# Kernel tuning notes

Hardware: AMD Instinct MI355X
Metric: run time of the kernel (lower is better)

## Reference

```python
import jax, jax.numpy as jnp
import numpy as np
from jax import lax

B, C, H, W = 8, 192, 128, 128
NUM_HEADS = 4
EPS = 1e-12  # torch F.normalize eps


def setup_inputs() -> dict:
    key = jax.random.key(0)
    ks = jax.random.split(key, 5)
    s = 0.05
    x = jax.random.normal(ks[0], (B, C, H, W), dtype=jnp.float32)
    w_qkv = jax.random.normal(ks[1], (3 * C, C), dtype=jnp.float32) * s      # 1x1 conv, no bias
    w_dw = jax.random.normal(ks[2], (3 * C, 1, 3, 3), dtype=jnp.float32) * s  # depthwise 3x3
    temperature = jnp.ones((1, NUM_HEADS, 1, 1), dtype=jnp.float32)
    w_out = jax.random.normal(ks[3], (C, C), dtype=jnp.float32) * s          # 1x1 conv, no bias
    return {"x": x, "w_qkv": w_qkv, "w_dw": w_dw, "temperature": temperature, "w_out": w_out}


def _l2_normalize(t):
    # matches torch F.normalize(dim=-1): t / max(||t||_2, eps)
    n = jnp.sqrt(jnp.sum(t * t, axis=-1, keepdims=True))
    return t / jnp.maximum(n, EPS)


def reference(x, w_qkv, w_dw, temperature, w_out):
    b, c, h, w = x.shape
    hd = c // NUM_HEADS
    # 1x1 pointwise conv (no bias)
    qkv = jnp.einsum('bchw,oc->bohw', x, w_qkv)
    # depthwise 3x3 conv, padding=1, groups=3c
    qkv = lax.conv_general_dilated(
        qkv, w_dw, window_strides=(1, 1), padding='SAME',
        feature_group_count=3 * c,
        dimension_numbers=('NCHW', 'OIHW', 'NCHW'))
    q, k, v = jnp.split(qkv, 3, axis=1)
    # [b, heads, head_dim, h*w]
    q = q.reshape(b, NUM_HEADS, hd, h * w)
    k = k.reshape(b, NUM_HEADS, hd, h * w)
    v = v.reshape(b, NUM_HEADS, hd, h * w)
    q = _l2_normalize(q)
    k = _l2_normalize(k)
    # channel attention: [b, heads, hd, hd]
    attn = jax.nn.softmax(jnp.einsum('bhcn,bhdn->bhcd', q, k) * temperature, axis=-1)
    out = jnp.einsum('bhcd,bhdn->bhcn', attn, v).reshape(b, c, h, w)
    out = jnp.einsum('bchw,oc->bohw', out, w_out)
    return out
```

## Files before the change

kernel.cpp:

```cpp
#include <hip/hip_runtime.h>
#include <hip/hip_bf16.h>

typedef unsigned short u16;
typedef unsigned int u32;

constexpr int kHW  = 16384;
constexpr int kC   = 192;
constexpr int kC3  = 576;
constexpr int kHD  = 48;
constexpr int kB   = 8;
constexpr int kSCH = 16;

typedef __attribute__((ext_vector_type(8))) short bfx8;
typedef __attribute__((ext_vector_type(4))) float fx4;

__device__ __forceinline__ float bfu2f(u32 u) { return __uint_as_float(u << 16); }
__device__ __forceinline__ u16 f2bfu(float f) {
  u32 x = __float_as_uint(f);
  return (u16)((x + 0x7fffu + ((x >> 16) & 1u)) >> 16);
}
__device__ __forceinline__ u32 pack2(float a, float b) {
  union { __hip_bfloat162 h; u32 u; } cv;
  cv.h = __float22bfloat162_rn(make_float2(a, b));
  return cv.u;
}

__global__ __launch_bounds__(256) void cast_f32_bf16(
    const float* __restrict__ in, u16* __restrict__ out, int n) {
  int i = blockIdx.x * 256 + threadIdx.x;
  if (i < n) out[i] = f2bfu(in[i]);
}

template <bool IN_F32, bool OUT_BF16>
__global__ __launch_bounds__(256) void gemm_cn(
    const u16* __restrict__ Abase, long aStride,
    const void* __restrict__ Bbase, long bStride,
    void* __restrict__ OutBase, long oStride, int nOB) {
  const int nwg = (int)gridDim.x;
  const int wg = ((int)blockIdx.x & 7) * (nwg >> 3) + ((int)blockIdx.x >> 3);
  const int o0 = (wg % nOB) * 64;
  const int rest = wg / nOB;
  const int n0 = (rest & 63) * 256;
  const int b  = rest >> 6;

  const int t = threadIdx.x;
  const int lane = t & 63, wv = t >> 6;
  const int fr = lane & 15, fg = lane >> 4;

  __shared__ u16 As[64 * 64];
  __shared__ __align__(16) u32 Bs[32 * 260];

  const u16* A = Abase + (size_t)b * aStride;

  fx4 acc[4][4];
#pragma unroll
  for (int m = 0; m < 4; ++m)
#pragma unroll
    for (int n = 0; n < 4; ++n) acc[m][n] = (fx4){0.f, 0.f, 0.f, 0.f};

  for (int k0 = 0; k0 < kC; k0 += 64) {
    if (k0) __syncthreads();
#pragma unroll
    for (int i = 0; i < 2; ++i) {
      int idx = t + i * 256;
      int row = idx >> 3, sl = idx & 7;
      uint4 v = *(const uint4*)(A + (size_t)(o0 + row) * kC + k0 + sl * 8);
      *(uint4*)(As + row * 64 + ((sl ^ (row & 7)) * 8)) = v;
    }
    if constexpr (IN_F32) {
      const float* Bg = (const float*)Bbase + (size_t)b * bStride;
#pragma unroll
      for (int i = 0; i < 8; ++i) {
        int p = i * 4 + wv;
        int k = k0 + 2 * p;
        const float* s0 = Bg + (size_t)k * kHW + n0 + lane * 4;
        float4 a = *(const float4*)s0;
        float4 c = *(const float4*)(s0 + (size_t)kHW);
        *(uint4*)(&Bs[p * 260 + lane * 4]) = make_uint4(
            pack2(a.x, c.x), pack2(a.y, c.y), pack2(a.z, c.z), pack2(a.w, c.w));
      }
    } else {
      const u16* Bg = (const u16*)Bbase + (size_t)b * bStride;
#pragma unroll
      for (int i = 0; i < 8; ++i) {
        int p = i * 4 + wv;
        int k = k0 + 2 * p;
        const u16* s0 = Bg + (size_t)k * kHW + n0 + lane * 4;
        uint2 a = *(const uint2*)s0;
        uint2 c = *(const uint2*)(s0 + (size_t)kHW);
        u32 w0 = (a.x & 0xffffu) | (c.x << 16);
        u32 w1 = (a.x >> 16)     | (c.x & 0xffff0000u);
        u32 w2 = (a.y & 0xffffu) | (c.y << 16);
        u32 w3 = (a.y >> 16)     | (c.y & 0xffff0000u);
        *(uint4*)(&Bs[p * 260 + lane * 4]) = make_uint4(w0, w1, w2, w3);
      }
    }
    __syncthreads();
#pragma unroll
    for (int ks = 0; ks < 2; ++ks) {
      bfx8 af[4], bf[4];
#pragma unroll
      for (int m = 0; m < 4; ++m) {
        int row = m * 16 + fr;
        af[m] = *(const bfx8*)(As + row * 64 + (((ks * 4 + fg) ^ (row & 7)) * 8));
      }
#pragma unroll
      for (int nf = 0; nf < 4; ++nf) {
        int base = (ks * 16 + fg * 4) * 260 + wv * 64 + nf * 16 + fr;
        union { uint4 u; bfx8 f; } cv;
        cv.u = make_uint4(Bs[base], Bs[base + 260], Bs[base + 520], Bs[base + 780]);
        bf[nf] = cv.f;
      }
#pragma unroll
      for (int m = 0; m < 4; ++m)
#pragma unroll
        for (int n = 0; n < 4; ++n)
          acc[m][n] = __builtin_amdgcn_mfma_f32_16x16x32_bf16(af[m], bf[n], acc[m][n], 0, 0, 0);
    }
  }

  if constexpr (OUT_BF16) {
    u16* O = (u16*)OutBase + (size_t)b * oStride;
#pragma unroll
    for (int m = 0; m < 4; ++m)
#pragma unroll
      for (int n = 0; n < 4; ++n) {
        int col = n0 + wv * 64 + n * 16 + fr;
#pragma unroll
        for (int r = 0; r < 4; ++r)
          O[(size_t)(o0 + m * 16 + fg * 4 + r) * kHW + col] = f2bfu(acc[m][n][r]);
      }
  } else {
    float* O = (float*)OutBase + (size_t)b * oStride;
#pragma unroll
    for (int m = 0; m < 4; ++m)
#pragma unroll
      for (int n = 0; n < 4; ++n) {
        int col = n0 + wv * 64 + n * 16 + fr;
#pragma unroll
        for (int r = 0; r < 4; ++r)
          O[(size_t)(o0 + m * 16 + fg * 4 + r) * kHW + col] = acc[m][n][r];
      }
  }
}

__device__ __forceinline__ void load_row3(const u16* __restrict__ plane, int hh,
                                          int w8, float v[10]) {
  uint4 m = make_uint4(0u, 0u, 0u, 0u);
  if ((unsigned)hh <= 127u) m = *(const uint4*)(plane + hh * 128 + w8 * 8);
  u32 left  = __shfl_up(m.w >> 16, 1);
  u32 right = __shfl_down(m.x & 0xffffu, 1);
  v[1] = bfu2f(m.x & 0xffffu); v[2] = bfu2f(m.x >> 16);
  v[3] = bfu2f(m.y & 0xffffu); v[4] = bfu2f(m.y >> 16);
  v[5] = bfu2f(m.z & 0xffffu); v[6] = bfu2f(m.z >> 16);
  v[7] = bfu2f(m.w & 0xffffu); v[8] = bfu2f(m.w >> 16);
  v[0] = (w8 > 0)  ? bfu2f(left)  : 0.f;
  v[9] = (w8 < 15) ? bfu2f(right) : 0.f;
}

__global__ __launch_bounds__(256) void dwconv3x3_v3(
    const u16* __restrict__ in, const float* __restrict__ wdw,
    u16* __restrict__ out, float* __restrict__ ssqp) {
  const int bc = blockIdx.x;
  const int ch = bc % kC3;
  const int t = threadIdx.x;
  const int w8 = t & 15;
  const int h0 = (t >> 4) * 8;
  const u16* p = in + (size_t)bc * kHW;
  float wt[9];
#pragma unroll
  for (int j = 0; j < 9; ++j) wt[j] = wdw[ch * 9 + j];

  float v[3][10];
  load_row3(p, h0 - 1, w8, v[0]);
  load_row3(p, h0,     w8, v[1]);
  float ssq = 0.f;
  u16* op = out + (size_t)bc * kHW + h0 * 128 + w8 * 8;
#pragma unroll
  for (int r = 0; r < 8; ++r) {
    load_row3(p, h0 + r + 1, w8, v[(r + 2) % 3]);
    const float* r0 = v[r % 3];
    const float* r1 = v[(r + 1) % 3];
    const float* r2 = v[(r + 2) % 3];
    float o[8];
#pragma unroll
    for (int j = 0; j < 8; ++j) {
      o[j] = wt[0] * r0[j] + wt[1] * r0[j + 1] + wt[2] * r0[j + 2]
           + wt[3] * r1[j] + wt[4] * r1[j + 1] + wt[5] * r1[j + 2]
           + wt[6] * r2[j] + wt[7] * r2[j + 1] + wt[8] * r2[j + 2];
      ssq += o[j] * o[j];
    }
    *(uint4*)(op + r * 128) = make_uint4(pack2(o[0], o[1]), pack2(o[2], o[3]),
                                         pack2(o[4], o[5]), pack2(o[6], o[7]));
  }
  if (ch < 2 * kC) {
#pragma unroll
    for (int d = 1; d < 64; d <<= 1) ssq += __shfl_xor(ssq, d);
    __shared__ float red[4];
    if ((t & 63) == 0) red[t >> 6] = ssq;
    __syncthreads();
    if (t == 0) ssqp[bc] = red[0] + red[1] + red[2] + red[3];
  }
}

__global__ __launch_bounds__(256) void qk_mfma_lds(
    const u16* __restrict__ qkv2, float* __restrict__ Spart) {
  const int chunk = blockIdx.x;
  const int bh = blockIdx.y;
  const int b = bh >> 2, hh = bh & 3;
  const u16* qp = qkv2 + (size_t)(b * kC3 + hh * kHD) * kHW;
  const u16* kp = qp + (size_t)kC * kHW;

  __shared__ u16 smem[24576];
  u16* qs = smem;
  u16* ks = smem + 12288;
  float* sred = (float*)smem;

  const int t = threadIdx.x;
  const int wv = t >> 6, lane = t & 63;
  const int fr = lane & 15, fg = lane >> 4;

  fx4 acc[3][3];
#pragma unroll
  for (int i = 0; i < 3; ++i)
#pragma unroll
    for (int j = 0; j < 3; ++j) acc[i][j] = (fx4){0.f, 0.f, 0.f, 0.f};

  for (int round = 0; round < 4; ++round) {
    if (round) __syncthreads();
    const int nb = chunk * 1024 + round * 256;
#pragma unroll
    for (int j = 0; j < 6; ++j) {
      int idx = t + j * 256;
      int c = idx >> 5, sl = idx & 31;
      *(uint4*)(qs + c * 256 + ((sl ^ (c & 31)) * 8)) =
          *(const uint4*)(qp + (size_t)c * kHW + nb + sl * 8);
      *(uint4*)(ks + c * 256 + ((sl ^ (c & 31)) * 8)) =
          *(const uint4*)(kp + (size_t)c * kHW + nb + sl * 8);
    }
    __syncthreads();
#pragma unroll
    for (int s = 0; s < 2; ++s) {
      const int slot = wv * 8 + s * 4 + fg;
      bfx8 aq[3], ak[3];
#pragma unroll
      for (int tt = 0; tt < 3; ++tt) {
        int c = tt * 16 + fr;
        aq[tt] = *(const bfx8*)(qs + c * 256 + ((slot ^ (c & 31)) * 8));
        ak[tt] = *(const bfx8*)(ks + c * 256 + ((slot ^ (c & 31)) * 8));
      }
#pragma unroll
      for (int i = 0; i < 3; ++i)
#pragma unroll
        for (int j = 0; j < 3; ++j)
          acc[i][j] = __builtin_amdgcn_mfma_f32_16x16x32_bf16(aq[i], ak[j], acc[i][j], 0, 0, 0);
    }
  }

  __syncthreads();
  float* my = sred + wv * 2400;
#pragma unroll
  for (int i = 0; i < 3; ++i)
#pragma unroll
    for (int j = 0; j < 3; ++j)
#pragma unroll
      for (int r = 0; r < 4; ++r)
        my[(i * 16 + fg * 4 + r) * 50 + j * 16 + fr] = acc[i][j][r];
  __syncthreads();
  float* Sp = Spart + ((size_t)chunk * 32 + bh) * (kHD * kHD);
  for (int p = t; p < kHD * kHD; p += 256) {
    int idx = (p / kHD) * 50 + (p % kHD);
    Sp[p] = sred[idx] + sred[2400 + idx] + sred[4800 + idx] + sred[7200 + idx];
  }
}

__global__ __launch_bounds__(256) void attn_softmax(
    const float* __restrict__ Spart, const float* __restrict__ ssqp,
    const float* __restrict__ temp, float* __restrict__ attn) {
  const int bh = blockIdx.x, b = bh >> 2, hh = bh & 3;
  const int t = threadIdx.x;
  __shared__ float S[kHD * kHD];
  __shared__ float qn[kHD], kinv[kHD];
  for (int p = t; p < kHD * kHD; p += 256) {
    float s = 0.f;
#pragma unroll
    for (int c = 0; c < kSCH; ++c) s += Spart[((size_t)c * 32 + bh) * (kHD * kHD) + p];
    S[p] = s;
  }
  if (t < 48) {
    qn[t] = sqrtf(ssqp[b * kC3 + hh * kHD + t]);
  } else if (t < 96) {
    kinv[t - 48] = 1.f / fmaxf(sqrtf(ssqp[b * kC3 + kC + hh * kHD + (t - 48)]), 1e-12f);
  }
  __syncthreads();
  if (t < 48) {
    const float T = temp[hh];
    const float sqr = T / fmaxf(qn[t], 1e-12f);
    float m = -3.4e38f;
    for (int d = 0; d < kHD; ++d) {
      float v = S[t * kHD + d] * sqr * kinv[d];
      S[t * kHD + d] = v;
      m = fmaxf(m, v);
    }
    float sum = 0.f;
    for (int d = 0; d < kHD; ++d) {
      float e = expf(S[t * kHD + d] - m);
      S[t * kHD + d] = e;
      sum += e;
    }
    const float inv = 1.f / sum;
    float* A = attn + (size_t)bh * (kHD * kHD) + t * kHD;
    for (int d = 0; d < kHD; ++d) A[d] = S[t * kHD + d] * inv;
  }
}

__global__ __launch_bounds__(256) void make_m(
    const float* __restrict__ wout, const float* __restrict__ attn, u16* __restrict__ M) {
  int g = blockIdx.x * 256 + threadIdx.x;
  if (g >= kB * kC * kC) return;
  int j = g % kC;
  int o = (g / kC) % kC;
  int b = g / (kC * kC);
  int hh = j / kHD, d = j % kHD;
  const float* A = attn + (size_t)(b * 4 + hh) * (kHD * kHD) + d;
  const float* wo = wout + (size_t)o * kC + hh * kHD;
  float s = 0.f;
#pragma unroll
  for (int c = 0; c < kHD; ++c) s += wo[c] * A[c * kHD];
  M[g] = f2bfu(s);
}

extern "C" void kernel_launch(void* const* d_in, const int* in_sizes, int n_in,
                              void* d_out, int out_size, void* d_ws, size_t ws_size,
                              hipStream_t stream) {
  const float* x    = (const float*)d_in[0];
  const float* wqkv = (const float*)d_in[1];
  const float* wdw  = (const float*)d_in[2];
  const float* temp = (const float*)d_in[3];
  const float* wout = (const float*)d_in[4];

  size_t off = 0;
  u16* qkv1 = (u16*)((char*)d_ws + off); off += (size_t)kB * kC3 * kHW * 2;
  u16* qkv2 = (u16*)((char*)d_ws + off); off += (size_t)kB * kC3 * kHW * 2;
  u16* Wq   = (u16*)((char*)d_ws + off); off += (size_t)kC3 * kC * 2;
  float* ssqp = (float*)((char*)d_ws + off); off += (size_t)kB * kC3 * 4;
  if (off > ws_size) return;

  float* Spart = (float*)qkv1;
  float* attnb = Spart + (size_t)kSCH * 32 * kHD * kHD;
  u16*   Mb    = (u16*)(attnb + (size_t)32 * kHD * kHD);

  cast_f32_bf16<<<dim3((kC3 * kC + 255) / 256), 256, 0, stream>>>(wqkv, Wq, kC3 * kC);
  gemm_cn<true, true><<<dim3((kC3 / 64) * 64 * kB), 256, 0, stream>>>(
      Wq, 0L, (const void*)x, (long)kC * kHW, (void*)qkv1, (long)kC3 * kHW, kC3 / 64);
  dwconv3x3_v3<<<dim3(kB * kC3), 256, 0, stream>>>(qkv1, wdw, qkv2, ssqp);
  qk_mfma_lds<<<dim3(kSCH, 32), 256, 0, stream>>>(qkv2, Spart);
  attn_softmax<<<dim3(32), 256, 0, stream>>>(Spart, ssqp, temp, attnb);
  make_m<<<dim3((kB * kC * kC + 255) / 256), 256, 0, stream>>>(wout, attnb, Mb);
  gemm_cn<false, false><<<dim3((kC / 64) * 64 * kB), 256, 0, stream>>>(
      Mb, (long)kC * kC, (const void*)(qkv2 + (size_t)2 * kC * kHW),
      (long)kC3 * kHW, d_out, (long)kC * kHW, kC / 64);
}
```

Measured before the change: 278.9 us.

## Retile channel GEMMs to 192x128 tiles with 512-thread blocks for input reuse

Result: faster. 228.1 us (median of 2 runs) (-18.2%).

```diff
diff --git a/kernel.cpp b/kernel.cpp
--- a/kernel.cpp
+++ b/kernel.cpp
@@ -32,37 +32,38 @@
 }
 
 template <bool IN_F32, bool OUT_BF16>
-__global__ __launch_bounds__(256) void gemm_cn(
+__global__ __launch_bounds__(512, 4) void gemm_cn2(
     const u16* __restrict__ Abase, long aStride,
     const void* __restrict__ Bbase, long bStride,
     void* __restrict__ OutBase, long oStride, int nOB) {
   const int nwg = (int)gridDim.x;
   const int wg = ((int)blockIdx.x & 7) * (nwg >> 3) + ((int)blockIdx.x >> 3);
-  const int o0 = (wg % nOB) * 64;
+  const int o0 = (wg % nOB) * 192;
   const int rest = wg / nOB;
-  const int n0 = (rest & 63) * 256;
-  const int b  = rest >> 6;
+  const int n0 = (rest & 127) * 128;
+  const int b  = rest >> 7;
 
   const int t = threadIdx.x;
   const int lane = t & 63, wv = t >> 6;
+  const int wo = wv & 3, wn = wv >> 2;
   const int fr = lane & 15, fg = lane >> 4;
 
-  __shared__ u16 As[64 * 64];
-  __shared__ __align__(16) u32 Bs[32 * 260];
+  __shared__ u16 As[192 * 64];
+  __shared__ __align__(16) u32 Bs[32 * 132];
 
   const u16* A = Abase + (size_t)b * aStride;
 
-  fx4 acc[4][4];
-#pragma unroll
-  for (int m = 0; m < 4; ++m)
+  fx4 acc[3][4];
+#pragma unroll
+  for (int m = 0; m < 3; ++m)
 #pragma unroll
     for (int n = 0; n < 4; ++n) acc[m][n] = (fx4){0.f, 0.f, 0.f, 0.f};
 
   for (int k0 = 0; k0 < kC; k0 += 64) {
     if (k0) __syncthreads();
 #pragma unroll
-    for (int i = 0; i < 2; ++i) {
-      int idx = t + i * 256;
+    for (int i = 0; i < 3; ++i) {
+      int idx = t + i * 512;
       int row = idx >> 3, sl = idx & 7;
       uint4 v = *(const uint4*)(A + (size_t)(o0 + row) * kC + k0 + sl * 8);
       *(uint4*)(As + row * 64 + ((sl ^ (row & 7)) * 8)) = v;
@@ -70,49 +71,46 @@
     if constexpr (IN_F32) {
       const float* Bg = (const float*)Bbase + (size_t)b * bStride;
 #pragma unroll
-      for (int i = 0; i < 8; ++i) {
-        int p = i * 4 + wv;
-        int k = k0 + 2 * p;
-        const float* s0 = Bg + (size_t)k * kHW + n0 + lane * 4;
+      for (int i = 0; i < 2; ++i) {
+        int slot = t + i * 512;
+        int p = slot >> 5, nq = slot & 31;
+        const float* s0 = Bg + (size_t)(k0 + 2 * p) * kHW + n0 + nq * 4;
         float4 a = *(const float4*)s0;
         float4 c = *(const float4*)(s0 + (size_t)kHW);
-        *(uint4*)(&Bs[p * 260 + lane * 4]) = make_uint4(
+        *(uint4*)(&Bs[p * 132 + nq * 4]) = make_uint4(
             pack2(a.x, c.x), pack2(a.y, c.y), pack2(a.z, c.z), pack2(a.w, c.w));
       }
     } else {
       const u16* Bg = (const u16*)Bbase + (size_t)b * bStride;
-#pragma unroll
-      for (int i = 0; i < 8; ++i) {
-        int p = i * 4 + wv;
-        int k = k0 + 2 * p;
-        const u16* s0 = Bg + (size_t)k * kHW + n0 + lane * 4;
-        uint2 a = *(const uint2*)s0;
-        uint2 c = *(const uint2*)(s0 + (size_t)kHW);
-        u32 w0 = (a.x & 0xffffu) | (c.x << 16);
-        u32 w1 = (a.x >> 16)     | (c.x & 0xffff0000u);
-        u32 w2 = (a.y & 0xffffu) | (c.y << 16);
-        u32 w3 = (a.y >> 16)     | (c.y & 0xffff0000u);
-        *(uint4*)(&Bs[p * 260 + lane * 4]) = make_uint4(w0, w1, w2, w3);
-      }
+      int p = t >> 4, n8 = (t & 15) * 8;
+      const u16* s0 = Bg + (size_t)(k0 + 2 * p) * kHW + n0 + n8;
+      union { uint4 u; u16 h[8]; } a, c;
+      a.u = *(const uint4*)s0;
+      c.u = *(const uint4*)(s0 + (size_t)kHW);
+      u32 w[8];
+#pragma unroll
+      for (int j = 0; j < 8; ++j) w[j] = (u32)a.h[j] | ((u32)c.h[j] << 16);
+      *(uint4*)(&Bs[p * 132 + n8])     = make_uint4(w[0], w[1], w[2], w[3]);
+      *(uint4*)(&Bs[p * 132 + n8 + 4]) = make_uint4(w[4], w[5], w[6], w[7]);
     }
     __syncthreads();
 #pragma unroll
     for (int ks = 0; ks < 2; ++ks) {
-      bfx8 af[4], bf[4];
-#pragma unroll
-      for (int m = 0; m < 4; ++m) {
-        int row = m * 16 + fr;
+      bfx8 af[3], bf[4];
+#pragma unroll
+      for (int m = 0; m < 3; ++m) {
+        int row = wo * 48 + m * 16 + fr;
         af[m] = *(const bfx8*)(As + row * 64 + (((ks * 4 + fg) ^ (row & 7)) * 8));
       }
 #pragma unroll
       for (int nf = 0; nf < 4; ++nf) {
-        int base = (ks * 16 + fg * 4) * 260 + wv * 64 + nf * 16 + fr;
+        int base = (ks * 16 + fg * 4) * 132 + wn * 64 + nf * 16 + fr;
         union { uint4 u; bfx8 f; } cv;
-        cv.u = make_uint4(Bs[base], Bs[base + 260], Bs[base + 520], Bs[base + 780]);
+        cv.u = make_uint4(Bs[base], Bs[base + 132], Bs[base + 264], Bs[base + 396]);
         bf[nf] = cv.f;
       }
 #pragma unroll
-      for (int m = 0; m < 4; ++m)
+      for (int m = 0; m < 3; ++m)
 #pragma unroll
         for (int n = 0; n < 4; ++n)
           acc[m][n] = __builtin_amdgcn_mfma_f32_16x16x32_bf16(af[m], bf[n], acc[m][n], 0, 0, 0);
@@ -122,24 +120,24 @@
   if constexpr (OUT_BF16) {
     u16* O = (u16*)OutBase + (size_t)b * oStride;
 #pragma unroll
-    for (int m = 0; m < 4; ++m)
+    for (int m = 0; m < 3; ++m)
 #pragma unroll
       for (int n = 0; n < 4; ++n) {
-        int col = n0 + wv * 64 + n * 16 + fr;
+        int col = n0 + wn * 64 + n * 16 + fr;
 #pragma unroll
         for (int r = 0; r < 4; ++r)
-          O[(size_t)(o0 + m * 16 + fg * 4 + r) * kHW + col] = f2bfu(acc[m][n][r]);
+          O[(size_t)(o0 + wo * 48 + m * 16 + fg * 4 + r) * kHW + col] = f2bfu(acc[m][n][r]);
       }
   } else {
     float* O = (float*)OutBase + (size_t)b * oStride;
 #pragma unroll
-    for (int m = 0; m < 4; ++m)
+    for (int m = 0; m < 3; ++m)
 #pragma unroll
       for (int n = 0; n < 4; ++n) {
-        int col = n0 + wv * 64 + n * 16 + fr;
+        int col = n0 + wn * 64 + n * 16 + fr;
 #pragma unroll
         for (int r = 0; r < 4; ++r)
-          O[(size_t)(o0 + m * 16 + fg * 4 + r) * kHW + col] = acc[m][n][r];
+          O[(size_t)(o0 + wo * 48 + m * 16 + fg * 4 + r) * kHW + col] = acc[m][n][r];
       }
   }
 }
@@ -351,13 +349,13 @@
   u16*   Mb    = (u16*)(attnb + (size_t)32 * kHD * kHD);
 
   cast_f32_bf16<<<dim3((kC3 * kC + 255) / 256), 256, 0, stream>>>(wqkv, Wq, kC3 * kC);
-  gemm_cn<true, true><<<dim3((kC3 / 64) * 64 * kB), 256, 0, stream>>>(
-      Wq, 0L, (const void*)x, (long)kC * kHW, (void*)qkv1, (long)kC3 * kHW, kC3 / 64);
+  gemm_cn2<true, true><<<dim3(3 * 128 * kB), 512, 0, stream>>>(
+      Wq, 0L, (const void*)x, (long)kC * kHW, (void*)qkv1, (long)kC3 * kHW, 3);
   dwconv3x3_v3<<<dim3(kB * kC3), 256, 0, stream>>>(qkv1, wdw, qkv2, ssqp);
   qk_mfma_lds<<<dim3(kSCH, 32), 256, 0, stream>>>(qkv2, Spart);
   attn_softmax<<<dim3(32), 256, 0, stream>>>(Spart, ssqp, temp, attnb);
   make_m<<<dim3((kB * kC * kC + 255) / 256), 256, 0, stream>>>(wout, attnb, Mb);
-  gemm_cn<false, false><<<dim3((kC / 64) * 64 * kB), 256, 0, stream>>>(
+  gemm_cn2<false, false><<<dim3(1 * 128 * kB), 512, 0, stream>>>(
       Mb, (long)kC * kC, (const void*)(qkv2 + (size_t)2 * kC * kHW),
-      (long)kC3 * kHW, d_out, (long)kC * kHW, kC / 64);
-}
+      (long)kC3 * kHW, d_out, (long)kC * kHW, 1);
+}
```
